# Performance work log

Measured on AMD Instinct MI355X. Metric: run time of the kernel, lower is better.

## Reference

```python
import jax, jax.numpy as jnp
import numpy as np

EPS = 1e-5

def layernorm(x, w, b):
    mu = jnp.mean(x, axis=-1, keepdims=True)
    var = jnp.mean((x - mu) ** 2, axis=-1, keepdims=True)
    return (x - mu) / jnp.sqrt(var + EPS) * w + b

def setup_inputs() -> dict:
    key = jax.random.key(0)
    ks = jax.random.split(key, 20)
    N, E, G = 50000, 800000, 512
    IN, OUT, TXT, MAN = 128, 128, 768, 14
    d = {
        "x": jax.random.normal(ks[0], (N, IN), jnp.float32),
        "edge_index": jax.random.randint(ks[1], (2, E), 0, N),
        "batch": jnp.sort(jax.random.randint(ks[2], (N,), 0, G)),
        "batch_size": G,
        "text_embedding": jax.random.normal(ks[3], (G, TXT), jnp.float32),
        "features_embedding": jax.random.normal(ks[4], (G, MAN), jnp.float32),
        # params
        "ln_proj_w": jnp.ones((IN,)), "ln_proj_b": jnp.zeros((IN,)),
        "W_l": jax.random.normal(ks[5], (IN, OUT)) / np.sqrt(IN),
        "b_l": jnp.zeros((OUT,)),
        "W_r": jax.random.normal(ks[6], (IN, OUT)) / np.sqrt(IN),
        "ln_conv_w": jnp.ones((OUT,)), "ln_conv_b": jnp.zeros((OUT,)),
        "gate_w": jax.random.normal(ks[7], (OUT, 1)) / np.sqrt(OUT),
        "gate_b": jnp.zeros((1,)),
        "graph_weight": jnp.asarray(1.0, jnp.float32),
        "msg_W": jax.random.normal(ks[8], (TXT, OUT)) / np.sqrt(TXT),
        "msg_b": jnp.zeros((OUT,)),
        "feat_W": jax.random.normal(ks[9], (MAN, OUT)) / np.sqrt(MAN),
        "feat_b": jnp.zeros((OUT,)),
        "mixed_w": jnp.ones((3 * OUT,)), "mixed_b": jnp.zeros((3 * OUT,)),
        "fc1_W": jax.random.normal(ks[10], (3 * OUT, 1)) / np.sqrt(3 * OUT),
        "fc1_b": jnp.zeros((1,)),
    }
    return d

def reference(x, edge_index, batch, batch_size, text_embedding, features_embedding,
              ln_proj_w, ln_proj_b, W_l, b_l, W_r, ln_conv_w, ln_conv_b,
              gate_w, gate_b, graph_weight, msg_W, msg_b, feat_W, feat_b,
              mixed_w, mixed_b, fc1_W, fc1_b):
    N = x.shape[0]
    src, dst = edge_index[0], edge_index[1]
    # project_norm
    h = layernorm(x, ln_proj_w, ln_proj_b)
    # GraphSAGE (SAGEConv, mean aggregation): out = mean_j(h_j) @ W_l + b + h @ W_r
    msgs = h[src]                                   # [E, IN] gather
    agg = jax.ops.segment_sum(msgs, dst, num_segments=N)
    deg = jax.ops.segment_sum(jnp.ones((src.shape[0],), h.dtype), dst, num_segments=N)
    mean_nb = agg / jnp.maximum(deg, 1.0)[:, None]
    h = mean_nb @ W_l + b_l + h @ W_r
    # layernorm + gelu (HomogeneousGraphConvolution)
    h = jax.nn.gelu(layernorm(h, ln_conv_w, ln_conv_b), approximate=False)
    # AttentionalAggregation: scatter-softmax over `batch`
    gate = (h @ gate_w + gate_b)[:, 0]              # [N]
    seg_max = jax.ops.segment_max(gate, batch, num_segments=batch_size)
    seg_max = jnp.where(jnp.isfinite(seg_max), seg_max, 0.0)
    e = jnp.exp(gate - seg_max[batch])
    denom = jax.ops.segment_sum(e, batch, num_segments=batch_size)
    attn = (e / denom[batch])[:, None]              # [N,1]
    graph_embedding = jax.ops.segment_sum(attn * h, batch, num_segments=batch_size)
    # dropout is identity in eval mode
    weighted = graph_weight * graph_embedding
    msg_emb = jax.nn.gelu(text_embedding @ msg_W + msg_b, approximate=False)
    feat_emb = jax.nn.gelu(features_embedding @ feat_W + feat_b, approximate=False)
    emb = jnp.concatenate([weighted, msg_emb, feat_emb], axis=1)
    emb = layernorm(emb, mixed_w, mixed_b)
    logits = emb @ fc1_W + fc1_b
    return (logits, graph_embedding, attn)
```

## Files before the change

### kernel.cpp

```cpp
#include <hip/hip_runtime.h>


typedef unsigned short ushort_t;
typedef __attribute__((ext_vector_type(8))) short bf16x8;
typedef __attribute__((ext_vector_type(4))) float floatx4;

__device__ __forceinline__ float b2f(ushort_t u) {
    union { unsigned int i; float f; } v; v.i = ((unsigned int)u) << 16; return v.f;
}
__device__ __forceinline__ ushort_t f2b(float f) {
    union { float f; unsigned int i; } v; v.f = f;
    unsigned int x = v.i;
    return (ushort_t)((x + 0x7FFFu + ((x >> 16) & 1u)) >> 16);
}
__device__ __forceinline__ float gelu_f(float x) {
    return 0.5f * x * (1.0f + erff(x * 0.70710678118654752440f));
}
__device__ __forceinline__ float waveReduceSum(float v) {
#pragma unroll
    for (int o = 32; o; o >>= 1) v += __shfl_xor(v, o, 64);
    return v;
}
__device__ __forceinline__ float waveReduceMax(float v) {
#pragma unroll
    for (int o = 32; o; o >>= 1) v = fmaxf(v, __shfl_xor(v, o, 64));
    return v;
}

__global__ void k_prep(const float* __restrict__ Wl, const float* __restrict__ Wr,
                       ushort_t* __restrict__ Wt) {
    int id = blockIdx.x * 256 + threadIdx.x;
    if (id >= 32768) return;
    int n = id >> 8, k = id & 255;
    float v = (k < 128) ? Wl[k * 128 + n] : Wr[(k - 128) * 128 + n];
    Wt[n * 256 + k] = f2b(v);
}

__global__ void k_ln1(const float* __restrict__ x, const float* __restrict__ w,
                      const float* __restrict__ b, ushort_t* __restrict__ hb, int N) {
    int row  = (blockIdx.x * blockDim.x + threadIdx.x) >> 6;
    int lane = threadIdx.x & 63;
    if (row >= N) return;
    size_t base = (size_t)row * 128;
    float2 xv = ((const float2*)(x + base))[lane];
    float v0 = xv.x, v1 = xv.y;
    float s  = waveReduceSum(v0 + v1);
    float s2 = waveReduceSum(v0 * v0 + v1 * v1);
    float mu = s * (1.0f / 128.0f);
    float var = s2 * (1.0f / 128.0f) - mu * mu;
    float rstd = 1.0f / sqrtf(var + 1e-5f);
    int d = lane * 2;
    ushort2 ov;
    ov.x = f2b((v0 - mu) * rstd * w[d]     + b[d]);
    ov.y = f2b((v1 - mu) * rstd * w[d + 1] + b[d + 1]);
    ((ushort2*)(hb + base))[lane] = ov;
}

__global__ void k_deg(const int* __restrict__ ei, int* __restrict__ deg, int E) {
    int e = blockIdx.x * blockDim.x + threadIdx.x;
    if (e < E) atomicAdd(&deg[ei[E + e]], 1);
}

__global__ void k_chunksum(const int* __restrict__ deg, int* __restrict__ csum, int N) {
    int i = blockIdx.x * 256 + threadIdx.x;
    int v = (i < N) ? deg[i] : 0;
#pragma unroll
    for (int o = 32; o; o >>= 1) v += __shfl_xor(v, o, 64);
    __shared__ int buf[4];
    int lane = threadIdx.x & 63, wv = threadIdx.x >> 6;
    if (lane == 0) buf[wv] = v;
    __syncthreads();
    if (threadIdx.x == 0) csum[blockIdx.x] = buf[0] + buf[1] + buf[2] + buf[3];
}
__global__ void k_chunkscan(const int* __restrict__ csum, int* __restrict__ coff, int nch) {
    int t = threadIdx.x;
    int v = (t < nch) ? csum[t] : 0;
    __shared__ int sb[256];
    sb[t] = v; __syncthreads();
    for (int o = 1; o < 256; o <<= 1) {
        int a = (t >= o) ? sb[t - o] : 0;
        __syncthreads();
        sb[t] += a;
        __syncthreads();
    }
    coff[t] = sb[t] - v;
}
__global__ void k_cursor(const int* __restrict__ deg, const int* __restrict__ coff,
                         int* __restrict__ cursor, int N) {
    int t = threadIdx.x;
    int i = blockIdx.x * 256 + t;
    int v = (i < N) ? deg[i] : 0;
    __shared__ int sb[256];
    sb[t] = v; __syncthreads();
    for (int o = 1; o < 256; o <<= 1) {
        int a = (t >= o) ? sb[t - o] : 0;
        __syncthreads();
        sb[t] += a;
        __syncthreads();
    }
    if (i < N) cursor[i] = sb[t] - v + coff[blockIdx.x];
}

__global__ void k_scatter(const int* __restrict__ ei, int* __restrict__ cursor,
                          int* __restrict__ nbr, int E) {
    int e = blockIdx.x * blockDim.x + threadIdx.x;
    if (e >= E) return;
    int s = ei[e], d = ei[E + e];
    int pos = atomicAdd(&cursor[d], 1);
    nbr[pos] = s;
}

__global__ void k_aggcsr(const ushort_t* __restrict__ hb, const int* __restrict__ cursor,
                         const int* __restrict__ deg, const int* __restrict__ nbr,
                         ushort_t* __restrict__ meanb, int N) {
    int node = (blockIdx.x * blockDim.x + threadIdx.x) >> 6;
    int lane = threadIdx.x & 63;
    if (node >= N) return;
    int dg = deg[node];
    int st = cursor[node] - dg;
    float a0 = 0.f, a1 = 0.f;
    int j = 0;
    for (; j + 4 <= dg; j += 4) {
        int s0 = nbr[st + j],     s1 = nbr[st + j + 1];
        int s2 = nbr[st + j + 2], s3 = nbr[st + j + 3];
        ushort2 v0 = ((const ushort2*)(hb + (size_t)s0 * 128))[lane];
        ushort2 v1 = ((const ushort2*)(hb + (size_t)s1 * 128))[lane];
        ushort2 v2 = ((const ushort2*)(hb + (size_t)s2 * 128))[lane];
        ushort2 v3 = ((const ushort2*)(hb + (size_t)s3 * 128))[lane];
        a0 += b2f(v0.x) + b2f(v1.x) + b2f(v2.x) + b2f(v3.x);
        a1 += b2f(v0.y) + b2f(v1.y) + b2f(v2.y) + b2f(v3.y);
    }
    for (; j < dg; j++) {
        int s = nbr[st + j];
        ushort2 v = ((const ushort2*)(hb + (size_t)s * 128))[lane];
        a0 += b2f(v.x); a1 += b2f(v.y);
    }
    float inv = 1.0f / fmaxf((float)dg, 1.0f);
    ushort2 ov; ov.x = f2b(a0 * inv); ov.y = f2b(a1 * inv);
    ((ushort2*)(meanb + (size_t)node * 128))[lane] = ov;
}

__global__ void __launch_bounds__(256) k_gemm(
    const ushort_t* __restrict__ meanb, ushort_t* __restrict__ hb,
    const ushort_t* __restrict__ Wt, const float* __restrict__ bl,
    const float* __restrict__ lnw, const float* __restrict__ lnb,
    const float* __restrict__ gw, const float* __restrict__ gb,
    float* __restrict__ gate, int N) {
    __shared__ ushort_t A[16][264];
    __shared__ float H2[16][132];
    int t = threadIdx.x;
    int row0 = blockIdx.x * 16;
    {
        int r = t >> 4, i = t & 15;
        int row = row0 + r; if (row >= N) row = N - 1;
        *(bf16x8*)&A[r][i * 8]       = *(const bf16x8*)(meanb + (size_t)row * 128 + i * 8);
        *(bf16x8*)&A[r][128 + i * 8] = *(const bf16x8*)(hb    + (size_t)row * 128 + i * 8);
    }
    __syncthreads();
    int w = t >> 6, l = t & 63;
    int m16 = l & 15, quad = l >> 4;
    int n0 = w * 32 + m16;
    int n1 = n0 + 16;
    floatx4 acc0 = {0.f, 0.f, 0.f, 0.f}, acc1 = {0.f, 0.f, 0.f, 0.f};
    for (int ks = 0; ks < 256; ks += 32) {
        bf16x8 a  = *(const bf16x8*)&A[m16][ks + quad * 8];
        bf16x8 b0 = *(const bf16x8*)(Wt + (size_t)n0 * 256 + ks + quad * 8);
        bf16x8 b1 = *(const bf16x8*)(Wt + (size_t)n1 * 256 + ks + quad * 8);
        acc0 = __builtin_amdgcn_mfma_f32_16x16x32_bf16(a, b0, acc0, 0, 0, 0);
        acc1 = __builtin_amdgcn_mfma_f32_16x16x32_bf16(a, b1, acc1, 0, 0, 0);
    }
#pragma unroll
    for (int i = 0; i < 4; i++) {
        H2[quad * 4 + i][n0] = acc0[i];
        H2[quad * 4 + i][n1] = acc1[i];
    }
    __syncthreads();
    int d = l * 2;
    float bb0 = bl[d],  bb1 = bl[d + 1];
    float lw0 = lnw[d], lw1 = lnw[d + 1];
    float lb0 = lnb[d], lb1 = lnb[d + 1];
    float gw0 = gw[d],  gw1 = gw[d + 1];
    float gbias = gb[0];
#pragma unroll
    for (int rr = 0; rr < 4; rr++) {
        int r = w * 4 + rr;
        int row = row0 + r;
        if (row >= N) break;
        float v0 = H2[r][d] + bb0, v1 = H2[r][d + 1] + bb1;
        float s  = waveReduceSum(v0 + v1);
        float s2 = waveReduceSum(v0 * v0 + v1 * v1);
        float mu = s * (1.f / 128.f);
        float var = s2 * (1.f / 128.f) - mu * mu;
        float rstd = 1.0f / sqrtf(var + 1e-5f);
        float g0 = gelu_f((v0 - mu) * rstd * lw0 + lb0);
        float g1 = gelu_f((v1 - mu) * rstd * lw1 + lb1);
        float gp = waveReduceSum(g0 * gw0 + g1 * gw1);
        ushort2 ov; ov.x = f2b(g0); ov.y = f2b(g1);
        ((ushort2*)(hb + (size_t)row * 128))[l] = ov;
        if (l == 0) gate[row] = gp + gbias;
    }
}

__global__ void k_segstart(const int* __restrict__ batch, int* __restrict__ segstart,
                           int N, int G) {
    int i = blockIdx.x * blockDim.x + threadIdx.x;
    if (i >= N) return;
    int b = batch[i];
    if (i == 0) {
        for (int g = 0; g <= b; g++) segstart[g] = 0;
    } else {
        int pb = batch[i - 1];
        for (int g = pb + 1; g <= b; g++) segstart[g] = i;
    }
    if (i == N - 1) {
        for (int g = b + 1; g <= G; g++) segstart[g] = N;
    }
}

__global__ void __launch_bounds__(128) k_attn(
    const float* __restrict__ gate, const ushort_t* __restrict__ h3b,
    const int* __restrict__ segstart,
    float* __restrict__ ge_out, float* __restrict__ attn_out, int G) {
    int g = blockIdx.x, t = threadIdx.x;
    int s0 = segstart[g], s1 = segstart[g + 1];
    if (s1 <= s0) {
        ge_out[(size_t)g * 128 + t] = 0.0f;
        return;
    }
    int lane = t & 63, wv = t >> 6;
    __shared__ float wbuf[2];
    __shared__ float pbuf[128];
    float m = -3.0e38f;
    for (int i = s0 + t; i < s1; i += 128) m = fmaxf(m, gate[i]);
    m = waveReduceMax(m);
    if (lane == 0) wbuf[wv] = m;
    __syncthreads();
    m = fmaxf(wbuf[0], wbuf[1]);
    __syncthreads();
    float dsum = 0.f;
    for (int i = s0 + t; i < s1; i += 128) dsum += expf(gate[i] - m);
    dsum = waveReduceSum(dsum);
    if (lane == 0) wbuf[wv] = dsum;
    __syncthreads();
    float inv = 1.0f / (wbuf[0] + wbuf[1]);
    float acc = 0.f;
    for (int base = s0; base < s1; base += 128) {
        int n = min(128, s1 - base);
        __syncthreads();
        if (t < n) {
            float p = expf(gate[base + t] - m) * inv;
            pbuf[t] = p;
            attn_out[base + t] = p;
        }
        __syncthreads();
        for (int j = 0; j < n; j++)
            acc += pbuf[j] * b2f(h3b[(size_t)(base + j) * 128 + t]);
    }
    ge_out[(size_t)g * 128 + t] = acc;
}

__global__ void __launch_bounds__(128) k_tail(
    const float* __restrict__ text, const float* __restrict__ feats,
    const float* __restrict__ msgW, const float* __restrict__ msgb,
    const float* __restrict__ featW, const float* __restrict__ featb,
    const float* __restrict__ gwt, const float* __restrict__ mixw,
    const float* __restrict__ mixb, const float* __restrict__ fc1W,
    const float* __restrict__ fc1b, const float* __restrict__ ge,
    float* __restrict__ logits, int G) {
    int g = blockIdx.x, t = threadIdx.x;
    __shared__ float txt[768];
    __shared__ float rbuf[4];
    for (int i = t; i < 768; i += 128) txt[i] = text[(size_t)g * 768 + i];
    __syncthreads();
    float am = msgb[t];
    for (int k = 0; k < 768; k += 4) {
        float4 a = *(const float4*)&txt[k];
        am += a.x * msgW[(k + 0) * 128 + t] + a.y * msgW[(k + 1) * 128 + t]
            + a.z * msgW[(k + 2) * 128 + t] + a.w * msgW[(k + 3) * 128 + t];
    }
    float me = gelu_f(am);
    float af = featb[t];
#pragma unroll
    for (int k = 0; k < 14; k++) af += feats[g * 14 + k] * featW[k * 128 + t];
    float fe = gelu_f(af);
    float e0 = gwt[0] * ge[(size_t)g * 128 + t];
    float ps = e0 + me + fe, ps2 = e0 * e0 + me * me + fe * fe;
    int lane = t & 63, w = t >> 6;
    float r1 = waveReduceSum(ps), r2 = waveReduceSum(ps2);
    if (lane == 0) { rbuf[w] = r1; rbuf[2 + w] = r2; }
    __syncthreads();
    float S = rbuf[0] + rbuf[1], S2 = rbuf[2] + rbuf[3];
    float mu = S * (1.f / 384.f);
    float var = S2 * (1.f / 384.f) - mu * mu;
    float rstd = 1.0f / sqrtf(var + 1e-5f);
    float n0 = (e0 - mu) * rstd * mixw[t]       + mixb[t];
    float n1 = (me - mu) * rstd * mixw[128 + t] + mixb[128 + t];
    float n2 = (fe - mu) * rstd * mixw[256 + t] + mixb[256 + t];
    float lp = n0 * fc1W[t] + n1 * fc1W[128 + t] + n2 * fc1W[256 + t];
    __syncthreads();
    float r3 = waveReduceSum(lp);
    if (lane == 0) rbuf[w] = r3;
    __syncthreads();
    if (t == 0) logits[g] = rbuf[0] + rbuf[1] + fc1b[0];
}

extern "C" void kernel_launch(void* const* d_in, const int* in_sizes, int n_in,
                              void* d_out, int out_size, void* d_ws, size_t ws_size,
                              hipStream_t stream) {
    const float* x     = (const float*)d_in[0];
    const int*   ei    = (const int*)d_in[1];
    const int*   batch = (const int*)d_in[2];
    const float* text  = (const float*)d_in[4];
    const float* feats = (const float*)d_in[5];
    const float* lnpw  = (const float*)d_in[6];
    const float* lnpb  = (const float*)d_in[7];
    const float* Wl    = (const float*)d_in[8];
    const float* bl    = (const float*)d_in[9];
    const float* Wr    = (const float*)d_in[10];
    const float* lncw  = (const float*)d_in[11];
    const float* lncb  = (const float*)d_in[12];
    const float* gatew = (const float*)d_in[13];
    const float* gateb = (const float*)d_in[14];
    const float* gwt   = (const float*)d_in[15];
    const float* msgW  = (const float*)d_in[16];
    const float* msgb  = (const float*)d_in[17];
    const float* featW = (const float*)d_in[18];
    const float* featb = (const float*)d_in[19];
    const float* mixw  = (const float*)d_in[20];
    const float* mixb  = (const float*)d_in[21];
    const float* fc1W  = (const float*)d_in[22];
    const float* fc1b  = (const float*)d_in[23];

    int N = in_sizes[0] / 128;
    int E = in_sizes[1] / 2;
    int G = in_sizes[4] / 768;

    char* wp = (char*)d_ws;
    auto alloc = [&](size_t bytes) -> char* {
        char* p = wp; wp += (bytes + 255) & ~(size_t)255; return p;
    };
    ushort_t* hb    = (ushort_t*)alloc((size_t)N * 128 * 2);
    ushort_t* meanb = (ushort_t*)alloc((size_t)N * 128 * 2);
    ushort_t* Wt    = (ushort_t*)alloc(128 * 256 * 2);
    float*    gate  = (float*)alloc((size_t)N * 4);
    int*      deg   = (int*)alloc((size_t)N * 4);
    int*      cursor= (int*)alloc((size_t)N * 4);
    int*      nbr   = (int*)alloc((size_t)E * 4);
    int*      csum  = (int*)alloc(1024 * 4);
    int*      coff  = (int*)alloc(1024 * 4);
    int*      segst = (int*)alloc((size_t)(G + 2) * 4);

    float* logits_out = (float*)d_out;
    float* ge_out     = logits_out + G;
    float* attn_out   = ge_out + (size_t)G * 128;

    int nch = (N + 255) / 256;

    hipMemsetAsync(deg, 0, (size_t)N * 4, stream);

    k_prep     <<<128,               256, 0, stream>>>(Wl, Wr, Wt);
    k_ln1      <<<(N + 3) / 4,       256, 0, stream>>>(x, lnpw, lnpb, hb, N);
    k_deg      <<<(E + 255) / 256,   256, 0, stream>>>(ei, deg, E);
    k_chunksum <<<nch,               256, 0, stream>>>(deg, csum, N);
    k_chunkscan<<<1,                 256, 0, stream>>>(csum, coff, nch);
    k_cursor   <<<nch,               256, 0, stream>>>(deg, coff, cursor, N);
    k_scatter  <<<(E + 255) / 256,   256, 0, stream>>>(ei, cursor, nbr, E);
    k_aggcsr   <<<(N + 3) / 4,       256, 0, stream>>>(hb, cursor, deg, nbr, meanb, N);
    k_gemm     <<<(N + 15) / 16,     256, 0, stream>>>(meanb, hb, Wt, bl, lncw, lncb,
                                                       gatew, gateb, gate, N);
    k_segstart <<<(N + 255) / 256,   256, 0, stream>>>(batch, segst, N, G);
    k_attn     <<<G,                 128, 0, stream>>>(gate, hb, segst, ge_out, attn_out, G);
    k_tail     <<<G,                 128, 0, stream>>>(text, feats, msgW, msgb, featW, featb,
                                                       gwt, mixw, mixb, fc1W, fc1b,
                                                       ge_out, logits_out, G);
}
```

Baseline: 324.6 us.

## Build CSR via two-level bucketed scatter with shared-memory local sort

```diff
diff --git a/kernel.cpp b/kernel.cpp
--- a/kernel.cpp
+++ b/kernel.cpp
@@ -101,13 +101,42 @@
     if (i < N) cursor[i] = sb[t] - v + coff[blockIdx.x];
 }
 
-__global__ void k_scatter(const int* __restrict__ ei, int* __restrict__ cursor,
-                          int* __restrict__ nbr, int E) {
+__global__ void k_binit(const int* __restrict__ cursor, int* __restrict__ bcur,
+                        int nb, int N, int E) {
+    int b = blockIdx.x * blockDim.x + threadIdx.x;
+    if (b > nb) return;
+    int node = b << 7;
+    bcur[b] = (node < N) ? cursor[node] : E;
+}
+
+__global__ void k_bscatter(const int* __restrict__ ei, int* __restrict__ bcur,
+                           unsigned int* __restrict__ packed, int E) {
     int e = blockIdx.x * blockDim.x + threadIdx.x;
     if (e >= E) return;
     int s = ei[e], d = ei[E + e];
-    int pos = atomicAdd(&cursor[d], 1);
-    nbr[pos] = s;
+    int pos = atomicAdd(&bcur[d >> 7], 1);
+    packed[pos] = ((unsigned int)(d & 127) << 25) | (unsigned int)s;
+}
+
+__global__ void __launch_bounds__(256) k_bsort(
+    const unsigned int* __restrict__ packed, const int* __restrict__ cursor,
+    int* __restrict__ nbr, int N, int E) {
+    __shared__ int lcur[128];
+    int b = blockIdx.x, t = threadIdx.x;
+    int node0 = b << 7;
+    if (t < 128) {
+        int node = node0 + t;
+        lcur[t] = (node < N) ? cursor[node] : 0;
+    }
+    __syncthreads();
+    int gstart = cursor[node0];
+    int next = node0 + 128;
+    int gend = (next < N) ? cursor[next] : E;
+    for (int i = gstart + t; i < gend; i += 256) {
+        unsigned int p = packed[i];
+        int pos = atomicAdd(&lcur[p >> 25], 1);
+        nbr[pos] = (int)(p & 0x1FFFFFFu);
+    }
 }
 
 __global__ void k_aggcsr(const ushort_t* __restrict__ hb, const int* __restrict__ cursor,
@@ -117,7 +146,7 @@
     int lane = threadIdx.x & 63;
     if (node >= N) return;
     int dg = deg[node];
-    int st = cursor[node] - dg;
+    int st = cursor[node];
     float a0 = 0.f, a1 = 0.f;
     int j = 0;
     for (; j + 4 <= dg; j += 4) {
@@ -339,22 +368,25 @@
     auto alloc = [&](size_t bytes) -> char* {
         char* p = wp; wp += (bytes + 255) & ~(size_t)255; return p;
     };
-    ushort_t* hb    = (ushort_t*)alloc((size_t)N * 128 * 2);
-    ushort_t* meanb = (ushort_t*)alloc((size_t)N * 128 * 2);
-    ushort_t* Wt    = (ushort_t*)alloc(128 * 256 * 2);
-    float*    gate  = (float*)alloc((size_t)N * 4);
-    int*      deg   = (int*)alloc((size_t)N * 4);
-    int*      cursor= (int*)alloc((size_t)N * 4);
-    int*      nbr   = (int*)alloc((size_t)E * 4);
-    int*      csum  = (int*)alloc(1024 * 4);
-    int*      coff  = (int*)alloc(1024 * 4);
-    int*      segst = (int*)alloc((size_t)(G + 2) * 4);
+    ushort_t* hb     = (ushort_t*)alloc((size_t)N * 128 * 2);
+    ushort_t* meanb  = (ushort_t*)alloc((size_t)N * 128 * 2);
+    ushort_t* Wt     = (ushort_t*)alloc(128 * 256 * 2);
+    float*    gate   = (float*)alloc((size_t)N * 4);
+    int*      deg    = (int*)alloc((size_t)N * 4);
+    int*      cursor = (int*)alloc((size_t)N * 4);
+    int*      nbr    = (int*)alloc((size_t)E * 4);
+    unsigned int* packed = (unsigned int*)alloc((size_t)E * 4);
+    int*      csum   = (int*)alloc(1024 * 4);
+    int*      coff   = (int*)alloc(1024 * 4);
+    int*      bcur   = (int*)alloc(4096 * 4);
+    int*      segst  = (int*)alloc((size_t)(G + 2) * 4);
 
     float* logits_out = (float*)d_out;
     float* ge_out     = logits_out + G;
     float* attn_out   = ge_out + (size_t)G * 128;
 
     int nch = (N + 255) / 256;
+    int nb  = (N + 127) / 128;
 
     hipMemsetAsync(deg, 0, (size_t)N * 4, stream);
 
@@ -364,7 +396,9 @@
     k_chunksum <<<nch,               256, 0, stream>>>(deg, csum, N);
     k_chunkscan<<<1,                 256, 0, stream>>>(csum, coff, nch);
     k_cursor   <<<nch,               256, 0, stream>>>(deg, coff, cursor, N);
-    k_scatter  <<<(E + 255) / 256,   256, 0, stream>>>(ei, cursor, nbr, E);
+    k_binit    <<<(nb + 256) / 256,  256, 0, stream>>>(cursor, bcur, nb, N, E);
+    k_bscatter <<<(E + 255) / 256,   256, 0, stream>>>(ei, bcur, packed, E);
+    k_bsort    <<<nb,                256, 0, stream>>>(packed, cursor, nbr, N, E);
     k_aggcsr   <<<(N + 3) / 4,       256, 0, stream>>>(hb, cursor, deg, nbr, meanb, N);
     k_gemm     <<<(N + 15) / 16,     256, 0, stream>>>(meanb, hb, Wt, bl, lncw, lncb,
                                                        gatew, gateb, gate, N);
```

After: 559.2 us. +72.3%, slower.
